# Kernel optimization log

Hardware: AMD Instinct MI355X
Metric: run time of the kernel (lower is better)

## Reference

```python
import jax, jax.numpy as jnp
import numpy as np

B, T, DIM, NH = 2, 2048, 1024, 16
HD = DIM // NH  # 64


def setup_inputs() -> dict:
    key = jax.random.key(0)
    ks = jax.random.split(key, 5)
    x = jax.random.normal(ks[0], (B, T, DIM), dtype=jnp.float32)
    # realistic RoPE tables (any float tables work; use true rotary angles)
    inv_freq = 1.0 / (10000.0 ** (jnp.arange(0, HD, 2, dtype=jnp.float32) / HD))  # [HD/2]
    ang = jnp.arange(T, dtype=jnp.float32)[:, None] * inv_freq[None, :]           # [T, HD/2]
    ang = jnp.repeat(ang, 2, axis=-1)                                             # [T, HD] interleaved pairs
    sin = jnp.sin(ang)[None, None]  # [1,1,T,HD]
    cos = jnp.cos(ang)[None, None]
    W_qkv = jax.random.normal(ks[1], (DIM, 3 * DIM), dtype=jnp.float32) * (DIM ** -0.5)
    W_proj = jax.random.normal(ks[2], (DIM, DIM), dtype=jnp.float32) * (DIM ** -0.5)
    return {"x": x, "sin": sin, "cos": cos, "W_qkv": W_qkv, "W_proj": W_proj}


def _rope(x, sin, cos):
    # x: [B,H,T,D]; sin/cos: [1,1,T,D]
    x1, x2 = x[..., ::2], x[..., 1::2]
    xr = jnp.stack((-x2, x1), axis=-1).reshape(x.shape)  # interleave (-x2, x1)
    return x * cos + xr * sin


def reference(x, sin, cos, W_qkv, W_proj):
    Bx, Tx, C = x.shape
    nh, hd = NH, C // NH
    qkv = x @ W_qkv                                   # [B,T,3C]
    q, k, v = jnp.split(qkv, 3, axis=-1)
    to_bhtd = lambda t: t.reshape(Bx, Tx, nh, hd).transpose(0, 2, 1, 3)
    q, k, v = to_bhtd(q), to_bhtd(k), to_bhtd(v)      # [B,H,T,D]
    q = _rope(q, sin[:, :, :Tx], cos[:, :, :Tx])
    k = _rope(k, sin[:, :, :Tx], cos[:, :, :Tx])
    scale = 1.0 / jnp.sqrt(jnp.asarray(hd, dtype=x.dtype))
    scores = jnp.einsum('bhqd,bhkd->bhqk', q, k) * scale
    causal = jnp.tril(jnp.ones((Tx, Tx), dtype=bool))
    scores = jnp.where(causal, scores, jnp.finfo(scores.dtype).min)
    attn = jax.nn.softmax(scores, axis=-1)
    y = jnp.einsum('bhqk,bhkd->bhqd', attn, v)        # [B,H,T,D]
    y = y.transpose(0, 2, 1, 3).reshape(Bx, Tx, C)
    return y @ W_proj
```

## Files before the change

kernel.cpp:

```cpp
#include <hip/hip_runtime.h>


typedef float  f32x4  __attribute__((ext_vector_type(4)));
typedef __bf16 bf16x8 __attribute__((ext_vector_type(8)));
typedef short  short8 __attribute__((ext_vector_type(8)));

#define Bb   2
#define Tt   2048
#define DIMc 1024
#define NHh  16
#define HDd  64

__device__ __forceinline__ short f2bf(float f) {
    unsigned u = __builtin_bit_cast(unsigned, f);
    u += 0x7fffu + ((u >> 16) & 1u);
    return (short)(u >> 16);
}

__device__ __forceinline__ f32x4 mfma16(short8 a, short8 b, f32x4 c) {
    return __builtin_amdgcn_mfma_f32_16x16x32_bf16(
        __builtin_bit_cast(bf16x8, a), __builtin_bit_cast(bf16x8, b), c, 0, 0, 0);
}

__device__ __forceinline__ void gl_lds16(const void* g, void* l) {
    __builtin_amdgcn_global_load_lds(
        (const __attribute__((address_space(1))) unsigned int*)g,
        (__attribute__((address_space(3))) unsigned int*)l, 16, 0, 0);
}

__global__ __launch_bounds__(256) void convX(const float* __restrict__ X,
                                             short* __restrict__ Xb)
{
    size_t i = ((size_t)blockIdx.x * 256 + threadIdx.x) * 8;
    float4 a = *(const float4*)(X + i);
    float4 b = *(const float4*)(X + i + 4);
    short8 s;
    s[0] = f2bf(a.x); s[1] = f2bf(a.y); s[2] = f2bf(a.z); s[3] = f2bf(a.w);
    s[4] = f2bf(b.x); s[5] = f2bf(b.y); s[6] = f2bf(b.z); s[7] = f2bf(b.w);
    *(short8*)(Xb + i) = s;
}

__global__ __launch_bounds__(256) void convT(const float* __restrict__ W,
                                             short* __restrict__ Wt, int N)
{
    __shared__ float L[64][65];
    const int kb = blockIdx.x * 64, nb = blockIdx.y * 64;
    const int tid = threadIdx.x;
#pragma unroll
    for (int it = 0; it < 4; it++) {
        int kk = it * 16 + (tid >> 4), c = (tid & 15) * 4;
        float4 v = *(const float4*)(W + (size_t)(kb + kk) * N + nb + c);
        L[c + 0][kk] = v.x; L[c + 1][kk] = v.y;
        L[c + 2][kk] = v.z; L[c + 3][kk] = v.w;
    }
    __syncthreads();
#pragma unroll
    for (int it = 0; it < 2; it++) {
        int n = it * 32 + (tid >> 3), ks = (tid & 7) * 8;
        short8 s;
#pragma unroll
        for (int j = 0; j < 8; j++) s[j] = f2bf(L[n][ks + j]);
        *(short8*)(Wt + (size_t)(nb + n) * 1024 + kb + ks) = s;
    }
}

__global__ __launch_bounds__(256) void qkv_rope(
    const short* __restrict__ A, const short* __restrict__ Bt,
    const float* __restrict__ Sn, const float* __restrict__ Cs,
    short* __restrict__ Qo, short* __restrict__ Ko, short* __restrict__ Vt)
{
    __shared__ __align__(16) short As[128][32];
    __shared__ __align__(16) short Bs[128][32];
    const int bm = blockIdx.x, bn = blockIdx.y;
    const int tid = threadIdx.x;
    const int wv = tid >> 6, lane = tid & 63, g = lane >> 4, l16 = lane & 15;
    const int wr = wv >> 1, wc = wv & 1;

    f32x4 acc[4][4];
#pragma unroll
    for (int i = 0; i < 4; i++)
#pragma unroll
        for (int j = 0; j < 4; j++) acc[i][j] = (f32x4){0.f, 0.f, 0.f, 0.f};

    const int rA = tid >> 2, cA = (tid & 3) << 3;
    for (int k0 = 0; k0 < 1024; k0 += 32) {
#pragma unroll
        for (int i = 0; i < 2; i++)
            gl_lds16(A + (size_t)(bm * 128 + i * 64 + rA) * 1024 + k0 + cA,
                     &As[i * 64 + rA][cA]);
#pragma unroll
        for (int i = 0; i < 2; i++)
            gl_lds16(Bt + (size_t)(bn * 128 + i * 64 + rA) * 1024 + k0 + cA,
                     &Bs[i * 64 + rA][cA]);
        __syncthreads();
        short8 af[4], bfr[4];
#pragma unroll
        for (int mt = 0; mt < 4; mt++) af[mt]  = *(const short8*)&As[wr * 64 + mt * 16 + l16][g * 8];
#pragma unroll
        for (int nt = 0; nt < 4; nt++) bfr[nt] = *(const short8*)&Bs[wc * 64 + nt * 16 + l16][g * 8];
#pragma unroll
        for (int mt = 0; mt < 4; mt++)
#pragma unroll
            for (int nt = 0; nt < 4; nt++) acc[mt][nt] = mfma16(af[mt], bfr[nt], acc[mt][nt]);
        __syncthreads();
    }

#pragma unroll
    for (int mt = 0; mt < 4; mt++)
#pragma unroll
        for (int nt = 0; nt < 4; nt++)
#pragma unroll
            for (int r = 0; r < 4; r++) {
                int m = bm * 128 + wr * 64 + mt * 16 + g * 4 + r;
                int n = bn * 128 + wc * 64 + nt * 16 + l16;
                float val = acc[mt][nt][r];
                float partner = __shfl_xor(val, 1, 64);
                int b = m >> 11, t = m & 2047;
                int sec = n >> 10, nn = n & 1023;
                int h = nn >> 6, d = nn & 63;
                if (sec == 2) {
                    Vt[(((size_t)(b * 16 + h) * 64 + d) << 11) + t] = f2bf(val);
                } else {
                    float sv = Sn[t * 64 + d], cv = Cs[t * 64 + d];
                    float ro = (d & 1) ? fmaf(val, cv, partner * sv)
                                       : fmaf(val, cv, -partner * sv);
                    short* dst = (sec == 0) ? Qo : Ko;
                    dst[(((size_t)(b * 16 + h) << 11) + t) * 64 + d] = f2bf(ro);
                }
            }
}

__global__ __launch_bounds__(256, 4) void attn(
    const short* __restrict__ Q, const short* __restrict__ K,
    const short* __restrict__ V, short* __restrict__ Y)
{
    __shared__ __align__(16) short Ks[2][64][64];
    __shared__ __align__(16) short Vs[2][64][64];
    __shared__ __align__(16) short Pl[4][16][64];

    const int id = blockIdx.y * gridDim.x + blockIdx.x;
    const int bh = id >> 5;
    const int qi = ((id & 31) + ((id >> 8) << 3)) & 31;
    const int tid = threadIdx.x, wv = tid >> 6, lane = tid & 63;
    const int g = lane >> 4, l16 = lane & 15;
    const int q0w = qi * 64 + wv * 16;
    const short* Qb = Q + (size_t)bh * Tt * 64;
    const short* Kb = K + (size_t)bh * Tt * 64;
    const short* Vb = V + (size_t)bh * 64 * Tt;

    const int rj = lane >> 3, cc = lane & 7, gc = cc ^ rj;

    auto stage = [&](int s, int buf) {
        int k0s = s * 64;
#pragma unroll
        for (int j = 0; j < 2; j++) {
            int row = wv * 16 + j * 8 + rj;
            gl_lds16(Kb + (size_t)(k0s + row) * 64 + gc * 8, &Ks[buf][row][cc << 3]);
        }
#pragma unroll
        for (int j = 0; j < 2; j++) {
            int row = wv * 16 + j * 8 + rj;
            gl_lds16(Vb + (size_t)row * Tt + k0s + gc * 8, &Vs[buf][row][cc << 3]);
        }
    };

    short8 qf[2];
#pragma unroll
    for (int ss = 0; ss < 2; ss++)
        qf[ss] = *(const short8*)(Qb + (size_t)(q0w + l16) * 64 + ss * 32 + g * 8);

    f32x4 o[4];
#pragma unroll
    for (int nt = 0; nt < 4; nt++) o[nt] = (f32x4){0.f, 0.f, 0.f, 0.f};
    float lsum[4] = {0.f, 0.f, 0.f, 0.f};

    const int nsteps = qi + 1;
    const int sw = l16 & 7;

    stage(0, 0);
    __syncthreads();

    for (int s = 0; s < nsteps; ++s) {
        if (s + 1 < nsteps) stage(s + 1, (s + 1) & 1);
        const int kb = s & 1, k0 = s * 64;

        f32x4 S[4];
#pragma unroll
        for (int t = 0; t < 4; t++) {
            S[t] = (f32x4){0.f, 0.f, 0.f, 0.f};
#pragma unroll
            for (int ss = 0; ss < 2; ss++) {
                short8 kf = *(const short8*)&Ks[kb][t * 16 + l16][((ss * 4 + g) ^ sw) << 3];
                S[t] = mfma16(qf[ss], kf, S[t]);
            }
        }

        float p[4][4];
        if (s < nsteps - 1) {
#pragma unroll
            for (int t = 0; t < 4; t++)
#pragma unroll
                for (int r = 0; r < 4; r++)
                    p[t][r] = __expf(fmaf(S[t][r], 0.125f, -10.f));
        } else {
#pragma unroll
            for (int t = 0; t < 4; t++)
#pragma unroll
                for (int r = 0; r < 4; r++) {
                    int key = k0 + t * 16 + l16, qq = q0w + g * 4 + r;
                    p[t][r] = (key <= qq) ? __expf(fmaf(S[t][r], 0.125f, -10.f)) : 0.f;
                }
        }
#pragma unroll
        for (int r = 0; r < 4; r++)
            lsum[r] += (p[0][r] + p[1][r]) + (p[2][r] + p[3][r]);

#pragma unroll
        for (int t = 0; t < 4; t++)
#pragma unroll
            for (int r = 0; r < 4; r++) {
                int row = g * 4 + r, c = t * 16 + l16;
                Pl[wv][row][(((c >> 3) ^ (row & 7)) << 3) | (c & 7)] = f2bf(p[t][r]);
            }
        asm volatile("" ::: "memory");
        short8 pf[2];
#pragma unroll
        for (int ks = 0; ks < 2; ks++)
            pf[ks] = *(const short8*)&Pl[wv][l16][((ks * 4 + g) ^ sw) << 3];
#pragma unroll
        for (int nt = 0; nt < 4; nt++)
#pragma unroll
            for (int ks = 0; ks < 2; ks++) {
                short8 vf = *(const short8*)&Vs[kb][nt * 16 + l16][((ks * 4 + g) ^ sw) << 3];
                o[nt] = mfma16(pf[ks], vf, o[nt]);
            }
        __syncthreads();
    }

    float inv[4];
#pragma unroll
    for (int r = 0; r < 4; r++) {
        float t = lsum[r];
        t += __shfl_xor(t, 1, 64);
        t += __shfl_xor(t, 2, 64);
        t += __shfl_xor(t, 4, 64);
        t += __shfl_xor(t, 8, 64);
        inv[r] = 1.0f / t;
    }
    const int b = bh >> 4, h = bh & 15;
#pragma unroll
    for (int nt = 0; nt < 4; nt++)
#pragma unroll
        for (int r = 0; r < 4; r++) {
            int qq = q0w + g * 4 + r, d = nt * 16 + l16;
            Y[((size_t)(b * Tt + qq)) * DIMc + h * 64 + d] = f2bf(o[nt][r] * inv[r]);
        }
}

__global__ __launch_bounds__(256) void proj(
    const short* __restrict__ A, const short* __restrict__ Bt, float* __restrict__ O)
{
    __shared__ __align__(16) short As[128][32];
    __shared__ __align__(16) short Bs[128][32];
    const int bm = blockIdx.x, bn = blockIdx.y;
    const int tid = threadIdx.x;
    const int wv = tid >> 6, lane = tid & 63, g = lane >> 4, l16 = lane & 15;
    const int wr = wv >> 1, wc = wv & 1;

    f32x4 acc[4][4];
#pragma unroll
    for (int i = 0; i < 4; i++)
#pragma unroll
        for (int j = 0; j < 4; j++) acc[i][j] = (f32x4){0.f, 0.f, 0.f, 0.f};

    const int rA = tid >> 2, cA = (tid & 3) << 3;
    for (int k0 = 0; k0 < 1024; k0 += 32) {
#pragma unroll
        for (int i = 0; i < 2; i++)
            gl_lds16(A + (size_t)(bm * 128 + i * 64 + rA) * 1024 + k0 + cA,
                     &As[i * 64 + rA][cA]);
#pragma unroll
        for (int i = 0; i < 2; i++)
            gl_lds16(Bt + (size_t)(bn * 128 + i * 64 + rA) * 1024 + k0 + cA,
                     &Bs[i * 64 + rA][cA]);
        __syncthreads();
        short8 af[4], bfr[4];
#pragma unroll
        for (int mt = 0; mt < 4; mt++) af[mt]  = *(const short8*)&As[wr * 64 + mt * 16 + l16][g * 8];
#pragma unroll
        for (int nt = 0; nt < 4; nt++) bfr[nt] = *(const short8*)&Bs[wc * 64 + nt * 16 + l16][g * 8];
#pragma unroll
        for (int mt = 0; mt < 4; mt++)
#pragma unroll
            for (int nt = 0; nt < 4; nt++) acc[mt][nt] = mfma16(af[mt], bfr[nt], acc[mt][nt]);
        __syncthreads();
    }

#pragma unroll
    for (int mt = 0; mt < 4; mt++)
#pragma unroll
        for (int nt = 0; nt < 4; nt++)
#pragma unroll
            for (int r = 0; r < 4; r++) {
                int m = bm * 128 + wr * 64 + mt * 16 + g * 4 + r;
                int n = bn * 128 + wc * 64 + nt * 16 + l16;
                O[(size_t)m * 1024 + n] = acc[mt][nt][r];
            }
}

extern "C" void kernel_launch(void* const* d_in, const int* in_sizes, int n_in,
                              void* d_out, int out_size, void* d_ws, size_t ws_size,
                              hipStream_t stream)
{
    const float* x     = (const float*)d_in[0];
    const float* sn    = (const float*)d_in[1];
    const float* cs    = (const float*)d_in[2];
    const float* wqkv  = (const float*)d_in[3];
    const float* wproj = (const float*)d_in[4];
    float* out = (float*)d_out;

    char* ws = (char*)d_ws;
    const size_t MB = 1024 * 1024;
    short* q   = (short*)(ws);
    short* k   = (short*)(ws + 8  * MB);
    short* vt  = (short*)(ws + 16 * MB);
    short* y   = (short*)(ws + 24 * MB);
    short* xb  = (short*)(ws + 32 * MB);
    short* wqt = (short*)(ws + 40 * MB);
    short* wpt = (short*)(ws + 46 * MB);

    convX<<<2048, 256, 0, stream>>>(x, xb);
    convT<<<dim3(16, 48), 256, 0, stream>>>(wqkv, wqt, 3072);
    convT<<<dim3(16, 16), 256, 0, stream>>>(wproj, wpt, 1024);
    qkv_rope<<<dim3(32, 24), 256, 0, stream>>>(xb, wqt, sn, cs, q, k, vt);
    attn<<<dim3(Tt / 64, Bb * NHh), 256, 0, stream>>>(q, k, vt, y);
    proj<<<dim3(32, 8), 256, 0, stream>>>(y, wpt, out);
}
```

Measured before the change: 204.4 us.

## Double-buffer LDS staging in GEMMs and coalesce transposed V stores

Result: no change. 208.2 us (+1.9%).

```diff
diff --git a/kernel.cpp b/kernel.cpp
--- a/kernel.cpp
+++ b/kernel.cpp
@@ -69,8 +69,8 @@
     const float* __restrict__ Sn, const float* __restrict__ Cs,
     short* __restrict__ Qo, short* __restrict__ Ko, short* __restrict__ Vt)
 {
-    __shared__ __align__(16) short As[128][32];
-    __shared__ __align__(16) short Bs[128][32];
+    __shared__ __align__(16) short As[2][128][32];
+    __shared__ __align__(16) short Bs[2][128][32];
     const int bm = blockIdx.x, bn = blockIdx.y;
     const int tid = threadIdx.x;
     const int wv = tid >> 6, lane = tid & 63, g = lane >> 4, l16 = lane & 15;
@@ -83,51 +83,85 @@
         for (int j = 0; j < 4; j++) acc[i][j] = (f32x4){0.f, 0.f, 0.f, 0.f};
 
     const int rA = tid >> 2, cA = (tid & 3) << 3;
+    const short* pA = A  + (size_t)(bm * 128 + rA) * 1024 + cA;
+    const short* pB = Bt + (size_t)(bn * 128 + rA) * 1024 + cA;
+
+    auto stage = [&](int k0, int b) {
+        gl_lds16(pA + k0,             &As[b][rA][cA]);
+        gl_lds16(pA + k0 + 64 * 1024, &As[b][64 + rA][cA]);
+        gl_lds16(pB + k0,             &Bs[b][rA][cA]);
+        gl_lds16(pB + k0 + 64 * 1024, &Bs[b][64 + rA][cA]);
+    };
+
+    stage(0, 0);
+    __syncthreads();
+    int buf = 0;
     for (int k0 = 0; k0 < 1024; k0 += 32) {
-#pragma unroll
-        for (int i = 0; i < 2; i++)
-            gl_lds16(A + (size_t)(bm * 128 + i * 64 + rA) * 1024 + k0 + cA,
-                     &As[i * 64 + rA][cA]);
-#pragma unroll
-        for (int i = 0; i < 2; i++)
-            gl_lds16(Bt + (size_t)(bn * 128 + i * 64 + rA) * 1024 + k0 + cA,
-                     &Bs[i * 64 + rA][cA]);
-        __syncthreads();
+        if (k0 + 32 < 1024) stage(k0 + 32, buf ^ 1);
         short8 af[4], bfr[4];
 #pragma unroll
-        for (int mt = 0; mt < 4; mt++) af[mt]  = *(const short8*)&As[wr * 64 + mt * 16 + l16][g * 8];
-#pragma unroll
-        for (int nt = 0; nt < 4; nt++) bfr[nt] = *(const short8*)&Bs[wc * 64 + nt * 16 + l16][g * 8];
+        for (int mt = 0; mt < 4; mt++) af[mt]  = *(const short8*)&As[buf][wr * 64 + mt * 16 + l16][g * 8];
+#pragma unroll
+        for (int nt = 0; nt < 4; nt++) bfr[nt] = *(const short8*)&Bs[buf][wc * 64 + nt * 16 + l16][g * 8];
 #pragma unroll
         for (int mt = 0; mt < 4; mt++)
 #pragma unroll
             for (int nt = 0; nt < 4; nt++) acc[mt][nt] = mfma16(af[mt], bfr[nt], acc[mt][nt]);
         __syncthreads();
-    }
-
-#pragma unroll
-    for (int mt = 0; mt < 4; mt++)
-#pragma unroll
-        for (int nt = 0; nt < 4; nt++)
-#pragma unroll
-            for (int r = 0; r < 4; r++) {
-                int m = bm * 128 + wr * 64 + mt * 16 + g * 4 + r;
-                int n = bn * 128 + wc * 64 + nt * 16 + l16;
-                float val = acc[mt][nt][r];
-                float partner = __shfl_xor(val, 1, 64);
-                int b = m >> 11, t = m & 2047;
-                int sec = n >> 10, nn = n & 1023;
-                int h = nn >> 6, d = nn & 63;
-                if (sec == 2) {
-                    Vt[(((size_t)(b * 16 + h) * 64 + d) << 11) + t] = f2bf(val);
-                } else {
+        buf ^= 1;
+    }
+
+    if (bn >= 16) {
+        short (*T)[136] = (short(*)[136])&As[0][0][0];
+        const int b  = bm >> 4;
+        const int t0 = (bm * 128) & 2047;
+        const int nbase = (bn - 16) * 128;
+#pragma unroll
+        for (int ch = 0; ch < 4; ++ch) {
+            __syncthreads();
+            if (wc == (ch >> 1)) {
+#pragma unroll
+                for (int ntl = 0; ntl < 2; ++ntl) {
+                    int nt = (ch & 1) * 2 + ntl;
+#pragma unroll
+                    for (int mt = 0; mt < 4; ++mt)
+#pragma unroll
+                        for (int r = 0; r < 4; ++r)
+                            T[ntl * 16 + l16][wr * 64 + mt * 16 + g * 4 + r] =
+                                f2bf(acc[mt][nt][r]);
+                }
+            }
+            __syncthreads();
+            int row = tid >> 3, c8 = (tid & 7) * 16;
+            int nn = nbase + ch * 32 + row;
+            int h = nn >> 6, d = nn & 63;
+            short8 v0 = *(const short8*)&T[row][c8];
+            short8 v1 = *(const short8*)&T[row][c8 + 8];
+            size_t base = (((size_t)(b * 16 + h) * 64 + d) << 11) + t0 + c8;
+            *(short8*)(Vt + base)     = v0;
+            *(short8*)(Vt + base + 8) = v1;
+        }
+    } else {
+#pragma unroll
+        for (int mt = 0; mt < 4; mt++)
+#pragma unroll
+            for (int nt = 0; nt < 4; nt++)
+#pragma unroll
+                for (int r = 0; r < 4; r++) {
+                    int m = bm * 128 + wr * 64 + mt * 16 + g * 4 + r;
+                    int n = bn * 128 + wc * 64 + nt * 16 + l16;
+                    float val = acc[mt][nt][r];
+                    float partner = __shfl_xor(val, 1, 64);
+                    int b = m >> 11, t = m & 2047;
+                    int sec = n >> 10, nn = n & 1023;
+                    int h = nn >> 6, d = nn & 63;
                     float sv = Sn[t * 64 + d], cv = Cs[t * 64 + d];
                     float ro = (d & 1) ? fmaf(val, cv, partner * sv)
                                        : fmaf(val, cv, -partner * sv);
                     short* dst = (sec == 0) ? Qo : Ko;
                     dst[(((size_t)(b * 16 + h) << 11) + t) * 64 + d] = f2bf(ro);
                 }
-            }
+    }
 }
 
 __global__ __launch_bounds__(256, 4) void attn(
@@ -260,8 +294,8 @@
 __global__ __launch_bounds__(256) void proj(
     const short* __restrict__ A, const short* __restrict__ Bt, float* __restrict__ O)
 {
-    __shared__ __align__(16) short As[128][32];
-    __shared__ __align__(16) short Bs[128][32];
+    __shared__ __align__(16) short As[2][128][32];
+    __shared__ __align__(16) short Bs[2][128][32];
     const int bm = blockIdx.x, bn = blockIdx.y;
     const int tid = threadIdx.x;
     const int wv = tid >> 6, lane = tid & 63, g = lane >> 4, l16 = lane & 15;
@@ -274,26 +308,32 @@
         for (int j = 0; j < 4; j++) acc[i][j] = (f32x4){0.f, 0.f, 0.f, 0.f};
 
     const int rA = tid >> 2, cA = (tid & 3) << 3;
+    const short* pA = A  + (size_t)(bm * 128 + rA) * 1024 + cA;
+    const short* pB = Bt + (size_t)(bn * 128 + rA) * 1024 + cA;
+
+    auto stage = [&](int k0, int b) {
+        gl_lds16(pA + k0,             &As[b][rA][cA]);
+        gl_lds16(pA + k0 + 64 * 1024, &As[b][64 + rA][cA]);
+        gl_lds16(pB + k0,             &Bs[b][rA][cA]);
+        gl_lds16(pB + k0 + 64 * 1024, &Bs[b][64 + rA][cA]);
+    };
+
+    stage(0, 0);
+    __syncthreads();
+    int buf = 0;
     for (int k0 = 0; k0 < 1024; k0 += 32) {
-#pragma unroll
-        for (int i = 0; i < 2; i++)
-            gl_lds16(A + (size_t)(bm * 128 + i * 64 + rA) * 1024 + k0 + cA,
-                     &As[i * 64 + rA][cA]);
-#pragma unroll
-        for (int i = 0; i < 2; i++)
-            gl_lds16(Bt + (size_t)(bn * 128 + i * 64 + rA) * 1024 + k0 + cA,
-                     &Bs[i * 64 + rA][cA]);
-        __syncthreads();
+        if (k0 + 32 < 1024) stage(k0 + 32, buf ^ 1);
         short8 af[4], bfr[4];
 #pragma unroll
-        for (int mt = 0; mt < 4; mt++) af[mt]  = *(const short8*)&As[wr * 64 + mt * 16 + l16][g * 8];
-#pragma unroll
-        for (int nt = 0; nt < 4; nt++) bfr[nt] = *(const short8*)&Bs[wc * 64 + nt * 16 + l16][g * 8];
+        for (int mt = 0; mt < 4; mt++) af[mt]  = *(const short8*)&As[buf][wr * 64 + mt * 16 + l16][g * 8];
+#pragma unroll
+        for (int nt = 0; nt < 4; nt++) bfr[nt] = *(const short8*)&Bs[buf][wc * 64 + nt * 16 + l16][g * 8];
 #pragma unroll
         for (int mt = 0; mt < 4; mt++)
 #pragma unroll
             for (int nt = 0; nt < 4; nt++) acc[mt][nt] = mfma16(af[mt], bfr[nt], acc[mt][nt]);
         __syncthreads();
+        buf ^= 1;
     }
 
 #pragma unroll
```

## Retile QKV and projection GEMMs with XOR-swizzled LDS and staged V transpose

Applied to the files above, without the earlier changes.

Result: faster. 188.0 us (-8.0%).

```diff
diff --git a/kernel.cpp b/kernel.cpp
--- a/kernel.cpp
+++ b/kernel.cpp
@@ -64,70 +64,106 @@
     }
 }
 
-__global__ __launch_bounds__(256) void qkv_rope(
+__global__ __launch_bounds__(256, 6) void qkv_rope(
     const short* __restrict__ A, const short* __restrict__ Bt,
     const float* __restrict__ Sn, const float* __restrict__ Cs,
     short* __restrict__ Qo, short* __restrict__ Ko, short* __restrict__ Vt)
 {
-    __shared__ __align__(16) short As[128][32];
-    __shared__ __align__(16) short Bs[128][32];
+    __shared__ __align__(16) short LP[64 * 64 + 128 * 64];
+    short (*As)[64] = (short(*)[64])LP;
+    short (*Bs)[64] = (short(*)[64])(LP + 64 * 64);
+
     const int bm = blockIdx.x, bn = blockIdx.y;
     const int tid = threadIdx.x;
     const int wv = tid >> 6, lane = tid & 63, g = lane >> 4, l16 = lane & 15;
     const int wr = wv >> 1, wc = wv & 1;
-
-    f32x4 acc[4][4];
-#pragma unroll
-    for (int i = 0; i < 4; i++)
+    const int sw = l16 & 7;
+
+    f32x4 acc[2][4];
+#pragma unroll
+    for (int i = 0; i < 2; i++)
 #pragma unroll
         for (int j = 0; j < 4; j++) acc[i][j] = (f32x4){0.f, 0.f, 0.f, 0.f};
 
-    const int rA = tid >> 2, cA = (tid & 3) << 3;
-    for (int k0 = 0; k0 < 1024; k0 += 32) {
-#pragma unroll
-        for (int i = 0; i < 2; i++)
-            gl_lds16(A + (size_t)(bm * 128 + i * 64 + rA) * 1024 + k0 + cA,
-                     &As[i * 64 + rA][cA]);
-#pragma unroll
-        for (int i = 0; i < 2; i++)
-            gl_lds16(Bt + (size_t)(bn * 128 + i * 64 + rA) * 1024 + k0 + cA,
-                     &Bs[i * 64 + rA][cA]);
-        __syncthreads();
-        short8 af[4], bfr[4];
-#pragma unroll
-        for (int mt = 0; mt < 4; mt++) af[mt]  = *(const short8*)&As[wr * 64 + mt * 16 + l16][g * 8];
-#pragma unroll
-        for (int nt = 0; nt < 4; nt++) bfr[nt] = *(const short8*)&Bs[wc * 64 + nt * 16 + l16][g * 8];
-#pragma unroll
-        for (int mt = 0; mt < 4; mt++)
-#pragma unroll
-            for (int nt = 0; nt < 4; nt++) acc[mt][nt] = mfma16(af[mt], bfr[nt], acc[mt][nt]);
-        __syncthreads();
-    }
-
-#pragma unroll
-    for (int mt = 0; mt < 4; mt++)
-#pragma unroll
-        for (int nt = 0; nt < 4; nt++)
-#pragma unroll
-            for (int r = 0; r < 4; r++) {
-                int m = bm * 128 + wr * 64 + mt * 16 + g * 4 + r;
-                int n = bn * 128 + wc * 64 + nt * 16 + l16;
-                float val = acc[mt][nt][r];
-                float partner = __shfl_xor(val, 1, 64);
-                int b = m >> 11, t = m & 2047;
-                int sec = n >> 10, nn = n & 1023;
-                int h = nn >> 6, d = nn & 63;
-                if (sec == 2) {
-                    Vt[(((size_t)(b * 16 + h) * 64 + d) << 11) + t] = f2bf(val);
-                } else {
+    const int sr = tid >> 3, c8 = tid & 7;
+    const int gc8 = (c8 ^ (sr & 7)) << 3;
+    const short* pA = A  + (size_t)(bm * 64  + sr) * 1024 + gc8;
+    const short* pB = Bt + (size_t)(bn * 128 + sr) * 1024 + gc8;
+
+    for (int k0 = 0; k0 < 1024; k0 += 64) {
+        gl_lds16(pA + k0,             &As[sr][c8 << 3]);
+        gl_lds16(pA + k0 + 32 * 1024, &As[32 + sr][c8 << 3]);
+        gl_lds16(pB + k0,             &Bs[sr][c8 << 3]);
+        gl_lds16(pB + k0 + 32 * 1024, &Bs[32 + sr][c8 << 3]);
+        gl_lds16(pB + k0 + 64 * 1024, &Bs[64 + sr][c8 << 3]);
+        gl_lds16(pB + k0 + 96 * 1024, &Bs[96 + sr][c8 << 3]);
+        __syncthreads();
+#pragma unroll
+        for (int ks = 0; ks < 2; ks++) {
+            short8 af[2], bfr[4];
+#pragma unroll
+            for (int mt = 0; mt < 2; mt++)
+                af[mt]  = *(const short8*)&As[wr * 32 + mt * 16 + l16][((ks * 4 + g) ^ sw) << 3];
+#pragma unroll
+            for (int nt = 0; nt < 4; nt++)
+                bfr[nt] = *(const short8*)&Bs[wc * 64 + nt * 16 + l16][((ks * 4 + g) ^ sw) << 3];
+#pragma unroll
+            for (int mt = 0; mt < 2; mt++)
+#pragma unroll
+                for (int nt = 0; nt < 4; nt++) acc[mt][nt] = mfma16(af[mt], bfr[nt], acc[mt][nt]);
+        }
+        __syncthreads();
+    }
+
+    if (bn >= 16) {
+        short (*T)[72] = (short(*)[72])LP;
+        const int b  = bm >> 5;
+        const int t0 = (bm * 64) & 2047;
+        const int nbase = (bn - 16) * 128;
+#pragma unroll
+        for (int ch = 0; ch < 4; ++ch) {
+            __syncthreads();
+            if (wc == (ch >> 1)) {
+#pragma unroll
+                for (int ntl = 0; ntl < 2; ++ntl) {
+                    int nt = (ch & 1) * 2 + ntl;
+#pragma unroll
+                    for (int mt = 0; mt < 2; ++mt)
+#pragma unroll
+                        for (int r = 0; r < 4; ++r)
+                            T[ntl * 16 + l16][wr * 32 + mt * 16 + g * 4 + r] =
+                                f2bf(acc[mt][nt][r]);
+                }
+            }
+            __syncthreads();
+            int row = tid >> 3, cc8 = (tid & 7) * 8;
+            int nn = nbase + ch * 32 + row;
+            int h = nn >> 6, d = nn & 63;
+            short8 v0 = *(const short8*)&T[row][cc8];
+            size_t base = (((size_t)(b * 16 + h) * 64 + d) << 11) + t0 + cc8;
+            *(short8*)(Vt + base) = v0;
+        }
+    } else {
+#pragma unroll
+        for (int mt = 0; mt < 2; mt++)
+#pragma unroll
+            for (int nt = 0; nt < 4; nt++)
+#pragma unroll
+                for (int r = 0; r < 4; r++) {
+                    int m = bm * 64 + wr * 32 + mt * 16 + g * 4 + r;
+                    int n = bn * 128 + wc * 64 + nt * 16 + l16;
+                    float val = acc[mt][nt][r];
+                    float partner = __shfl_xor(val, 1, 64);
+                    int b = m >> 11, t = m & 2047;
+                    int sec = n >> 10, nn = n & 1023;
+                    int h = nn >> 6, d = nn & 63;
                     float sv = Sn[t * 64 + d], cv = Cs[t * 64 + d];
                     float ro = (d & 1) ? fmaf(val, cv, partner * sv)
                                        : fmaf(val, cv, -partner * sv);
                     short* dst = (sec == 0) ? Qo : Ko;
                     dst[(((size_t)(b * 16 + h) << 11) + t) * 64 + d] = f2bf(ro);
                 }
-            }
+    }
 }
 
 __global__ __launch_bounds__(256, 4) void attn(
@@ -257,53 +293,59 @@
         }
 }
 
-__global__ __launch_bounds__(256) void proj(
+__global__ __launch_bounds__(256, 4) void proj(
     const short* __restrict__ A, const short* __restrict__ Bt, float* __restrict__ O)
 {
-    __shared__ __align__(16) short As[128][32];
-    __shared__ __align__(16) short Bs[128][32];
+    __shared__ __align__(16) short As[64][64];
+    __shared__ __align__(16) short Bs[64][64];
     const int bm = blockIdx.x, bn = blockIdx.y;
     const int tid = threadIdx.x;
     const int wv = tid >> 6, lane = tid & 63, g = lane >> 4, l16 = lane & 15;
     const int wr = wv >> 1, wc = wv & 1;
-
-    f32x4 acc[4][4];
-#pragma unroll
-    for (int i = 0; i < 4; i++)
-#pragma unroll
-        for (int j = 0; j < 4; j++) acc[i][j] = (f32x4){0.f, 0.f, 0.f, 0.f};
-
-    const int rA = tid >> 2, cA = (tid & 3) << 3;
-    for (int k0 = 0; k0 < 1024; k0 += 32) {
-#pragma unroll
-        for (int i = 0; i < 2; i++)
-            gl_lds16(A + (size_t)(bm * 128 + i * 64 + rA) * 1024 + k0 + cA,
-                     &As[i * 64 + rA][cA]);
-#pragma unroll
-        for (int i = 0; i < 2; i++)
-            gl_lds16(Bt + (size_t)(bn * 128 + i * 64 + rA) * 1024 + k0 + cA,
-                     &Bs[i * 64 + rA][cA]);
-        __syncthreads();
-        short8 af[4], bfr[4];
-#pragma unroll
-        for (int mt = 0; mt < 4; mt++) af[mt]  = *(const short8*)&As[wr * 64 + mt * 16 + l16][g * 8];
-#pragma unroll
-        for (int nt = 0; nt < 4; nt++) bfr[nt] = *(const short8*)&Bs[wc * 64 + nt * 16 + l16][g * 8];
-#pragma unroll
-        for (int mt = 0; mt < 4; mt++)
-#pragma unroll
-            for (int nt = 0; nt < 4; nt++) acc[mt][nt] = mfma16(af[mt], bfr[nt], acc[mt][nt]);
-        __syncthreads();
-    }
-
-#pragma unroll
-    for (int mt = 0; mt < 4; mt++)
-#pragma unroll
-        for (int nt = 0; nt < 4; nt++)
+    const int sw = l16 & 7;
+
+    f32x4 acc[2][2];
+#pragma unroll
+    for (int i = 0; i < 2; i++)
+#pragma unroll
+        for (int j = 0; j < 2; j++) acc[i][j] = (f32x4){0.f, 0.f, 0.f, 0.f};
+
+    const int sr = tid >> 3, c8 = tid & 7;
+    const int gc8 = (c8 ^ (sr & 7)) << 3;
+    const short* pA = A  + (size_t)(bm * 64 + sr) * 1024 + gc8;
+    const short* pB = Bt + (size_t)(bn * 64 + sr) * 1024 + gc8;
+
+    for (int k0 = 0; k0 < 1024; k0 += 64) {
+        gl_lds16(pA + k0,             &As[sr][c8 << 3]);
+        gl_lds16(pA + k0 + 32 * 1024, &As[32 + sr][c8 << 3]);
+        gl_lds16(pB + k0,             &Bs[sr][c8 << 3]);
+        gl_lds16(pB + k0 + 32 * 1024, &Bs[32 + sr][c8 << 3]);
+        __syncthreads();
+#pragma unroll
+        for (int ks = 0; ks < 2; ks++) {
+            short8 af[2], bfr[2];
+#pragma unroll
+            for (int mt = 0; mt < 2; mt++)
+                af[mt]  = *(const short8*)&As[wr * 32 + mt * 16 + l16][((ks * 4 + g) ^ sw) << 3];
+#pragma unroll
+            for (int nt = 0; nt < 2; nt++)
+                bfr[nt] = *(const short8*)&Bs[wc * 32 + nt * 16 + l16][((ks * 4 + g) ^ sw) << 3];
+#pragma unroll
+            for (int mt = 0; mt < 2; mt++)
+#pragma unroll
+                for (int nt = 0; nt < 2; nt++) acc[mt][nt] = mfma16(af[mt], bfr[nt], acc[mt][nt]);
+        }
+        __syncthreads();
+    }
+
+#pragma unroll
+    for (int mt = 0; mt < 2; mt++)
+#pragma unroll
+        for (int nt = 0; nt < 2; nt++)
 #pragma unroll
             for (int r = 0; r < 4; r++) {
-                int m = bm * 128 + wr * 64 + mt * 16 + g * 4 + r;
-                int n = bn * 128 + wc * 64 + nt * 16 + l16;
+                int m = bm * 64 + wr * 32 + mt * 16 + g * 4 + r;
+                int n = bn * 64 + wc * 32 + nt * 16 + l16;
                 O[(size_t)m * 1024 + n] = acc[mt][nt][r];
             }
 }
@@ -332,7 +374,7 @@
     convX<<<2048, 256, 0, stream>>>(x, xb);
     convT<<<dim3(16, 48), 256, 0, stream>>>(wqkv, wqt, 3072);
     convT<<<dim3(16, 16), 256, 0, stream>>>(wproj, wpt, 1024);
-    qkv_rope<<<dim3(32, 24), 256, 0, stream>>>(xb, wqt, sn, cs, q, k, vt);
+    qkv_rope<<<dim3(64, 24), 256, 0, stream>>>(xb, wqt, sn, cs, q, k, vt);
     attn<<<dim3(Tt / 64, Bb * NHh), 256, 0, stream>>>(q, k, vt, y);
-    proj<<<dim3(32, 8), 256, 0, stream>>>(y, wpt, out);
-}
+    proj<<<dim3(64, 16), 256, 0, stream>>>(y, wpt, out);
+}
```
